# Optimization experiments

Measured on AMD Instinct MI355X. Metric: run time of the kernel, lower is better.

The kernel has to match this reference:

```python
import jax, jax.numpy as jnp
import numpy as np

B, N, C, H = 8, 1024, 768, 12
D = C // H
HID = 4 * C
MAX_TEXT_LEN = 512
LN_EPS = 1e-5


def _ln(x, g, b):
    mu = jnp.mean(x, axis=-1, keepdims=True)
    var = jnp.mean(jnp.square(x - mu), axis=-1, keepdims=True)
    return (x - mu) * jax.lax.rsqrt(var + LN_EPS) * g + b


def _mlp(x, w1, b1, w2, b2):
    h = jax.nn.gelu(x @ w1.T + b1, approximate=False)
    return h @ w2.T + b2


def setup_inputs() -> dict:
    key = jax.random.key(0)
    ks = jax.random.split(key, 16)
    s = 0.02
    return {
        "x": jax.random.normal(ks[0], (B, N, C), jnp.float32),
        "mask": jax.random.randint(ks[1], (B, N), 0, 2).astype(bool),
        "rel_bias": jax.random.normal(ks[2], (H, N, N), jnp.float32) * s,
        "w_qkv": jax.random.normal(ks[3], (3 * C, C), jnp.float32) * s,
        "q_bias": jnp.zeros((C,), jnp.float32),
        "v_bias": jnp.zeros((C,), jnp.float32),
        "w_proj": jax.random.normal(ks[4], (C, C), jnp.float32) * s,
        "b_proj": jnp.zeros((C,), jnp.float32),
        "ln1_g": jnp.ones((C,), jnp.float32),
        "ln1_b": jnp.zeros((C,), jnp.float32),
        "ln2t_g": jnp.ones((C,), jnp.float32),
        "ln2t_b": jnp.zeros((C,), jnp.float32),
        "ln2i_g": jnp.ones((C,), jnp.float32),
        "ln2i_b": jnp.zeros((C,), jnp.float32),
        "w1t": jax.random.normal(ks[5], (HID, C), jnp.float32) * s,
        "b1t": jnp.zeros((HID,), jnp.float32),
        "w2t": jax.random.normal(ks[6], (C, HID), jnp.float32) * s,
        "b2t": jnp.zeros((C,), jnp.float32),
        "w1i": jax.random.normal(ks[7], (HID, C), jnp.float32) * s,
        "b1i": jnp.zeros((HID,), jnp.float32),
        "w2i": jax.random.normal(ks[8], (C, HID), jnp.float32) * s,
        "b2i": jnp.zeros((C,), jnp.float32),
        "gamma1": jnp.full((C,), 0.1, jnp.float32),
        "gamma2": jnp.full((C,), 0.1, jnp.float32),
    }


def reference(x, mask, rel_bias, w_qkv, q_bias, v_bias, w_proj, b_proj,
              ln1_g, ln1_b, ln2t_g, ln2t_b, ln2i_g, ln2i_b,
              w1t, b1t, w2t, b2t, w1i, b1i, w2i, b2i, gamma1, gamma2):
    # ---- attention branch ----
    h = _ln(x, ln1_g, ln1_b)
    qkv_bias = jnp.concatenate([q_bias, jnp.zeros_like(v_bias), v_bias])
    qkv = h @ w_qkv.T + qkv_bias                      # [B,N,3C]
    qkv = qkv.reshape(B, N, 3, H, D).transpose(2, 0, 3, 1, 4)  # [3,B,H,N,D]
    q, k, v = qkv[0], qkv[1], qkv[2]
    q = q * (D ** -0.5)
    attn = jnp.einsum('bhnd,bhmd->bhnm',
                      q.astype(jnp.float32), k.astype(jnp.float32))
    attn = attn + rel_bias[None]                      # [B,H,N,N]
    attn = jnp.where(mask[:, None, None, :], attn, -jnp.inf)
    attn = jax.nn.softmax(attn, axis=-1).astype(x.dtype)
    out = jnp.einsum('bhnm,bhmd->bhnd', attn, v)
    out = out.transpose(0, 2, 1, 3).reshape(B, N, C)
    out = out @ w_proj.T + b_proj
    x = x + gamma1 * out
    # ---- dual-branch layer-scaled MLP (mlp_vl is None path) ----
    xt = x[:, :MAX_TEXT_LEN]
    xi = x[:, MAX_TEXT_LEN:]
    xt = xt + gamma2 * _mlp(_ln(xt, ln2t_g, ln2t_b), w1t, b1t, w2t, b2t)
    xi = xi + gamma2 * _mlp(_ln(xi, ln2i_g, ln2i_b), w1i, b1i, w2i, b2i)
    return jnp.concatenate([xt, xi], axis=1)
```

## Files before the change

kernel.cpp:

```cpp
#include <hip/hip_runtime.h>
#include <hip/hip_bf16.h>
#include <math.h>

#define B_    8
#define N_TOK 1024
#define C_    768
#define H_    12
#define D_    64
#define HID_  3072

typedef __attribute__((ext_vector_type(4)))  float f32x4;
typedef __attribute__((ext_vector_type(16))) float f32x16;
typedef __attribute__((ext_vector_type(8)))  short s16x8;
typedef __attribute__((ext_vector_type(4)))  unsigned short u16x4;

static __device__ __forceinline__ unsigned short f2bf(float x){
  union { __hip_bfloat16 h; unsigned short u; } cv;
  cv.h = __float2bfloat16(x);
  return cv.u;
}
static __device__ __forceinline__ float bf2f(unsigned short u){
  return __uint_as_float(((unsigned)u) << 16);
}

#define GLOAD_LDS16(gp, lp) \
  __builtin_amdgcn_global_load_lds((const __attribute__((address_space(1))) unsigned int*)(gp), \
                                   (__attribute__((address_space(3))) unsigned int*)(lp), 16, 0, 0)

__global__ __launch_bounds__(256) void k_cvtall(
    const float* __restrict__ wq,  const float* __restrict__ wp,
    const float* __restrict__ w1t, const float* __restrict__ w2t,
    const float* __restrict__ w1i, const float* __restrict__ w2i,
    const float* __restrict__ bias,
    unsigned short* __restrict__ dq,  unsigned short* __restrict__ dp,
    unsigned short* __restrict__ d1t, unsigned short* __restrict__ d2t,
    unsigned short* __restrict__ d1i, unsigned short* __restrict__ d2i,
    unsigned short* __restrict__ db)
{
  int i = blockIdx.x * 256 + threadIdx.x;
  const float* src; unsigned short* dst; int o;
  if      (i <  442368){ src = wq;  dst = dq;  o = i; }
  else if (i <  589824){ src = wp;  dst = dp;  o = i -  442368; }
  else if (i < 1179648){ src = w1t; dst = d1t; o = i -  589824; }
  else if (i < 1769472){ src = w2t; dst = d2t; o = i - 1179648; }
  else if (i < 2359296){ src = w1i; dst = d1i; o = i - 1769472; }
  else if (i < 2949120){ src = w2i; dst = d2i; o = i - 2359296; }
  else                 { src = bias;dst = db;  o = i - 2949120; }
  float4 v = ((const float4*)src)[o];
  u16x4 r;
  r.x = f2bf(v.x); r.y = f2bf(v.y); r.z = f2bf(v.z); r.w = f2bf(v.w);
  *(u16x4*)(dst + (size_t)o*4) = r;
}

__global__ __launch_bounds__(256) void k_ln1(const float* __restrict__ x,
                                             const float* __restrict__ g,
                                             const float* __restrict__ bta,
                                             unsigned short* __restrict__ out){
  int row  = blockIdx.x*4 + (threadIdx.x >> 6);
  int lane = threadIdx.x & 63;
  const float* xr = x + (size_t)row*C_;
  float v[12]; float s = 0.f;
  #pragma unroll
  for (int i=0;i<12;i++){ v[i] = xr[lane + i*64]; s += v[i]; }
  #pragma unroll
  for (int m=1;m<64;m<<=1) s += __shfl_xor(s, m);
  float mu = s * (1.f/768.f);
  float vs = 0.f;
  #pragma unroll
  for (int i=0;i<12;i++){ float d = v[i]-mu; vs += d*d; }
  #pragma unroll
  for (int m=1;m<64;m<<=1) vs += __shfl_xor(vs, m);
  float rs = rsqrtf(vs*(1.f/768.f) + 1e-5f);
  unsigned short* orow = out + (size_t)row*C_;
  #pragma unroll
  for (int i=0;i<12;i++){ int c = lane + i*64; orow[c] = f2bf((v[i]-mu)*rs*g[c] + bta[c]); }
}

__global__ __launch_bounds__(256) void k_ln2(const float* __restrict__ xmid,
                                             const float* __restrict__ gt, const float* __restrict__ bt,
                                             const float* __restrict__ gi, const float* __restrict__ bi,
                                             unsigned short* __restrict__ outc){
  int row  = blockIdx.x*4 + (threadIdx.x >> 6);
  int lane = threadIdx.x & 63;
  int bb = row >> 10, n = row & 1023;
  const float* G = (n < 512) ? gt : gi;
  const float* Bb = (n < 512) ? bt : bi;
  int crow = (n < 512) ? (bb*512 + n) : (4096 + bb*512 + (n - 512));
  const float* xr = xmid + (size_t)row*C_;
  float v[12]; float s = 0.f;
  #pragma unroll
  for (int i=0;i<12;i++){ v[i] = xr[lane + i*64]; s += v[i]; }
  #pragma unroll
  for (int m=1;m<64;m<<=1) s += __shfl_xor(s, m);
  float mu = s * (1.f/768.f);
  float vs = 0.f;
  #pragma unroll
  for (int i=0;i<12;i++){ float d = v[i]-mu; vs += d*d; }
  #pragma unroll
  for (int m=1;m<64;m<<=1) vs += __shfl_xor(vs, m);
  float rs = rsqrtf(vs*(1.f/768.f) + 1e-5f);
  unsigned short* orow = outc + (size_t)crow*C_;
  #pragma unroll
  for (int i=0;i<12;i++){ int c = lane + i*64; orow[c] = f2bf((v[i]-mu)*rs*G[c] + Bb[c]); }
}

template<int MODE>
__global__ __launch_bounds__(256, 3) void k_gemm2(
    const unsigned short* __restrict__ A,
    const unsigned short* __restrict__ Bw0,
    const unsigned short* __restrict__ Bw1,
    int K,
    const float* __restrict__ bias0,
    const float* __restrict__ bias1,
    const float* __restrict__ qb2,
    const float* __restrict__ resid,
    const float* __restrict__ gamma,
    unsigned short* __restrict__ out_bf,
    float* __restrict__ out_f)
{
  __shared__ __align__(16) char smem[49152];
  const int tid = threadIdx.x;
  const int lane = tid & 63, w = tid >> 6;
  const int wr = w >> 1, wc = w & 1;
  const int l31 = lane & 31, h5 = lane >> 5;

  const int gx = gridDim.x;
  const int nwg = gx * gridDim.y;
  const int flat = blockIdx.y * gx + blockIdx.x;
  const int nid = (flat & 7) * (nwg >> 3) + (flat >> 3);
  const int bx = nid % gx, by = nid / gx;
  const int z = blockIdx.z;
  const int row0 = bx*128, col0 = by*128;

  const unsigned short* Ap = A;
  const unsigned short* Bp = Bw0;
  const float* bias = bias0;
  if (MODE == 2 || MODE == 3){
    if (z){ Ap = A + (size_t)4096*K; Bp = Bw1; bias = bias1; }
  }
  const char* Abase = (const char*)Ap;
  const char* Bbase = (const char*)Bp;
  const size_t rowbytes = (size_t)K*2;
  const int KT2 = K >> 5;

  auto stage = [&](int h, int slot_idx){
    char* slot = smem + slot_idx*16384;
    size_t kb = (size_t)h*64;
    #pragma unroll
    for (int it = 0; it < 2; it++){
      int L = it*4096 + tid*16;
      int r = L >> 6, cb = L & 63;
      int scb = cb ^ ((r & 6) << 3);
      GLOAD_LDS16(Abase + (size_t)(row0 + r)*rowbytes + kb + scb, slot + L);
    }
    #pragma unroll
    for (int it = 0; it < 2; it++){
      int L = it*4096 + tid*16;
      int r = L >> 6, cb = L & 63;
      int scb = cb ^ ((r & 6) << 3);
      GLOAD_LDS16(Bbase + (size_t)(col0 + r)*rowbytes + kb + scb, slot + 8192 + L);
    }
  };

  stage(0, 0); stage(1, 1);
  asm volatile("s_waitcnt vmcnt(4)" ::: "memory");
  __builtin_amdgcn_s_barrier();

  f32x16 acc[2][2] = {};
  int sh = 2;
  int sc_ = 0;
  for (int h = 0; h < KT2; h++){
    if (h + 2 < KT2){
      stage(h + 2, sh);
      sh = (sh == 2) ? 0 : sh + 1;
    }
    char* slot = smem + sc_*16384;
    sc_ = (sc_ == 2) ? 0 : sc_ + 1;
    s16x8 af[2][2], bfr[2][2];
    #pragma unroll
    for (int fm = 0; fm < 2; fm++){
      int ra = wr*64 + fm*32 + l31;
      int swa = (ra & 6) << 3;
      af[fm][0] = *(const s16x8*)(slot + ra*64 + ((h5*16) ^ swa));
      af[fm][1] = *(const s16x8*)(slot + ra*64 + ((32 + h5*16) ^ swa));
    }
    #pragma unroll
    for (int fn = 0; fn < 2; fn++){
      int rb = wc*64 + fn*32 + l31;
      int swb = (rb & 6) << 3;
      bfr[fn][0] = *(const s16x8*)(slot + 8192 + rb*64 + ((h5*16) ^ swb));
      bfr[fn][1] = *(const s16x8*)(slot + 8192 + rb*64 + ((32 + h5*16) ^ swb));
    }
    __builtin_amdgcn_s_setprio(1);
    #pragma unroll
    for (int kh = 0; kh < 2; kh++)
      #pragma unroll
      for (int fm = 0; fm < 2; fm++)
        #pragma unroll
        for (int fn = 0; fn < 2; fn++)
          acc[fm][fn] = __builtin_amdgcn_mfma_f32_32x32x16_bf16(af[fm][kh], bfr[fn][kh], acc[fm][fn], 0, 0, 0);
    __builtin_amdgcn_s_setprio(0);
    if (h + 1 < KT2){
      if (h + 2 < KT2) asm volatile("s_waitcnt vmcnt(4)" ::: "memory");
      else             asm volatile("s_waitcnt vmcnt(0)" ::: "memory");
      __builtin_amdgcn_s_barrier();
    }
  }

  const float QSCALE = 0.18033688011f;
  #pragma unroll
  for (int fm = 0; fm < 2; fm++){
    #pragma unroll
    for (int fn = 0; fn < 2; fn++){
      int j = col0 + wc*64 + fn*32 + l31;
      f32x16 a = acc[fm][fn];
      if (MODE == 0){
        int which = (j >= 1536) ? 2 : (j >= 768 ? 1 : 0);
        int cj = j - which*768;
        float bs = (which == 0) ? bias0[cj] : (which == 2 ? qb2[cj] : 0.f);
        int head = cj >> 6, d = cj & 63;
        #pragma unroll
        for (int r = 0; r < 16; r++){
          int m = row0 + wr*64 + fm*32 + (r & 3) + 8*(r >> 2) + 4*h5;
          int bb = m >> 10, n = m & 1023;
          float val = a[r] + bs;
          if (which == 0) val *= QSCALE;
          out_bf[((((size_t)which*B_ + bb)*H_ + head)*N_TOK + n)*D_ + d] = f2bf(val);
        }
      } else if (MODE == 1){
        float gm = gamma[j], bs = bias[j];
        #pragma unroll
        for (int r = 0; r < 16; r++){
          int m = row0 + wr*64 + fm*32 + (r & 3) + 8*(r >> 2) + 4*h5;
          size_t idx = (size_t)m*C_ + j;
          out_f[idx] = resid[idx] + gm*(a[r] + bs);
        }
      } else if (MODE == 2){
        float bs = bias[j];
        unsigned short* outp = out_bf + (size_t)z*4096*HID_;
        #pragma unroll
        for (int r = 0; r < 16; r++){
          int m = row0 + wr*64 + fm*32 + (r & 3) + 8*(r >> 2) + 4*h5;
          float t = a[r] + bs;
          outp[(size_t)m*HID_ + j] = f2bf(0.5f*t*(1.f + erff(t*0.70710678118654752f)));
        }
      } else {
        float gm = gamma[j], bs = bias[j];
        #pragma unroll
        for (int r = 0; r < 16; r++){
          int m = row0 + wr*64 + fm*32 + (r & 3) + 8*(r >> 2) + 4*h5;
          int bb = m >> 9, n = (m & 511) + (z ? 512 : 0);
          size_t idx = ((size_t)bb*N_TOK + n)*C_ + j;
          out_f[idx] = resid[idx] + gm*(a[r] + bs);
        }
      }
    }
  }
}

__global__ __launch_bounds__(256, 2) void k_attn(
    const unsigned short* __restrict__ qb,
    const unsigned short* __restrict__ kb,
    const unsigned short* __restrict__ vb,
    const unsigned short* __restrict__ bias_bf,
    const int* __restrict__ mask,
    unsigned short* __restrict__ outb)
{
  __shared__ __align__(16) char smem[45056];
  char* Vt0 = smem;
  char* Vt1 = smem + 8192;
  char* Ks  = smem + 16384;
  char* Bs  = smem + 24576;
  float* maskf = (float*)(smem + 40960);
  char* Oep = smem;

  int wg = blockIdx.x;
  int x = wg & 7, rest = wg >> 3;
  int qt = rest & 7, gl = rest >> 3;
  int g = gl*8 + x;
  int h = g % 12, bb = g / 12;

  const int tid = threadIdx.x, lane = tid & 63, w = tid >> 6;
  const int l31 = lane & 31, h5 = lane >> 5;
  const size_t bh = (size_t)bb*H_ + h;
  const char* qp = (const char*)(qb + bh*N_TOK*D_);
  const char* kp = (const char*)(kb + bh*N_TOK*D_);
  const unsigned short* vp = vb + bh*N_TOK*D_;
  const char* bp = (const char*)(bias_bf + (size_t)h*N_TOK*N_TOK);
  const int q0 = qt*128;
  const int qrow = q0 + w*32 + l31;
  const int qr = w*32 + l31;

  #pragma unroll
  for (int it = 0; it < 2; it++){
    int L = it*4096 + tid*16; int r = L >> 7, cb = L & 127;
    GLOAD_LDS16(kp + (size_t)r*128 + (cb ^ ((r & 7) << 4)), Ks + L);
  }
  #pragma unroll
  for (int it = 0; it < 4; it++){
    int L = it*4096 + tid*16; int r = L >> 7, cb = L & 127;
    GLOAD_LDS16(bp + (size_t)(q0 + r)*2048 + (cb ^ ((r & 7) << 4)), Bs + L);
  }
  unsigned short vv[16];
  #pragma unroll
  for (int j = 0; j < 16; j++) vv[j] = vp[(size_t)(w*16 + j)*D_ + lane];
  {
    int4 m4 = *(const int4*)(mask + bb*N_TOK + tid*4);
    float4 f4;
    f4.x = m4.x ? 0.f : -1e30f; f4.y = m4.y ? 0.f : -1e30f;
    f4.z = m4.z ? 0.f : -1e30f; f4.w = m4.w ? 0.f : -1e30f;
    *(float4*)(maskf + tid*4) = f4;
  }
  s16x8 qf[4];
  #pragma unroll
  for (int t = 0; t < 4; t++)
    qf[t] = *(const s16x8*)(qp + (size_t)qrow*128 + t*32 + h5*16);
  #pragma unroll
  for (int i = 0; i < 2; i++){
    s16x8 pk;
    #pragma unroll
    for (int e = 0; e < 8; e++) pk[e] = (short)vv[i*8 + e];
    *(s16x8*)(Vt0 + lane*128 + ((w*32 + i*16) ^ ((lane & 7) << 4))) = pk;
  }
  __syncthreads();

  f32x16 oacc[2] = {};
  float lrow = 0.f;

  for (int t = 0; t < 16; t++){
    const int kt = t*64;
    char* Vbuf = (t & 1) ? Vt1 : Vt0;
    char* Vnxt = (t & 1) ? Vt0 : Vt1;

    s16x8 kfr[2][4];
    #pragma unroll
    for (int ck = 0; ck < 2; ck++)
      #pragma unroll
      for (int tt = 0; tt < 4; tt++)
        kfr[ck][tt] = *(const s16x8*)(Ks + (ck*32 + l31)*128 + ((tt*32 + h5*16) ^ ((l31 & 7) << 4)));
    u16x4 bv[2][4];
    #pragma unroll
    for (int ck = 0; ck < 2; ck++)
      #pragma unroll
      for (int rq = 0; rq < 4; rq++){
        int off = ck*64 + rq*16 + h5*8;
        bv[ck][rq] = *(const u16x4*)(Bs + qr*128 + (off ^ ((qr & 7) << 4)));
      }
    __syncthreads();

    if (t < 15){
      #pragma unroll
      for (int it = 0; it < 2; it++){
        int L = it*4096 + tid*16; int r = L >> 7, cb = L & 127;
        GLOAD_LDS16(kp + (size_t)(kt + 64 + r)*128 + (cb ^ ((r & 7) << 4)), Ks + L);
      }
      #pragma unroll
      for (int it = 0; it < 4; it++){
        int L = it*4096 + tid*16; int r = L >> 7, cb = L & 127;
        GLOAD_LDS16(bp + (size_t)(q0 + r)*2048 + (size_t)(kt + 64)*2 + (cb ^ ((r & 7) << 4)), Bs + L);
      }
      #pragma unroll
      for (int j = 0; j < 16; j++)
        vv[j] = vp[(size_t)(kt + 64 + w*16 + j)*D_ + lane];
    }

    f32x16 sacc[2] = {};
    __builtin_amdgcn_s_setprio(1);
    #pragma unroll
    for (int tt = 0; tt < 4; tt++){
      sacc[0] = __builtin_amdgcn_mfma_f32_32x32x16_bf16(kfr[0][tt], qf[tt], sacc[0], 0, 0, 0);
      sacc[1] = __builtin_amdgcn_mfma_f32_32x32x16_bf16(kfr[1][tt], qf[tt], sacc[1], 0, 0, 0);
    }
    __builtin_amdgcn_s_setprio(0);

    float sv[2][16];
    float ps = 0.f;
    #pragma unroll
    for (int ck = 0; ck < 2; ck++){
      #pragma unroll
      for (int r = 0; r < 16; r++){
        int kk = ck*32 + (r & 3) + 8*(r >> 2) + 4*h5;
        float p = exp2f(fmaf(bf2f(bv[ck][r >> 2][r & 3]), 1.44269504089f,
                             sacc[ck][r] + maskf[kt + kk]));
        sv[ck][r] = p;
        ps += p;
      }
    }
    lrow += ps;

    #pragma unroll
    for (int ck = 0; ck < 2; ck++){
      #pragma unroll
      for (int kh = 0; kh < 2; kh++){
        unsigned wA, wB, wC, wD;
        asm("v_cvt_pk_bf16_f32 %0, %1, %2" : "=v"(wA) : "v"(sv[ck][kh*8+0]), "v"(sv[ck][kh*8+1]));
        asm("v_cvt_pk_bf16_f32 %0, %1, %2" : "=v"(wB) : "v"(sv[ck][kh*8+2]), "v"(sv[ck][kh*8+3]));
        asm("v_cvt_pk_bf16_f32 %0, %1, %2" : "=v"(wC) : "v"(sv[ck][kh*8+4]), "v"(sv[ck][kh*8+5]));
        asm("v_cvt_pk_bf16_f32 %0, %1, %2" : "=v"(wD) : "v"(sv[ck][kh*8+6]), "v"(sv[ck][kh*8+7]));
        unsigned tA = (unsigned)__shfl_xor((int)wA, 32);
        unsigned tB = (unsigned)__shfl_xor((int)wB, 32);
        unsigned tC = (unsigned)__shfl_xor((int)wC, 32);
        unsigned tD = (unsigned)__shfl_xor((int)wD, 32);
        union { unsigned u[4]; s16x8 v; } pu;
        pu.u[0] = h5 ? tC : wA;
        pu.u[1] = h5 ? tD : wB;
        pu.u[2] = h5 ? wC : tA;
        pu.u[3] = h5 ? wD : tB;
        __builtin_amdgcn_s_setprio(1);
        #pragma unroll
        for (int dt = 0; dt < 2; dt++){
          int d = dt*32 + l31;
          s16x8 vf = *(const s16x8*)(Vbuf + d*128 + ((ck*64 + kh*32 + h5*16) ^ ((d & 7) << 4)));
          oacc[dt] = __builtin_amdgcn_mfma_f32_32x32x16_bf16(vf, pu.v, oacc[dt], 0, 0, 0);
        }
        __builtin_amdgcn_s_setprio(0);
      }
    }

    if (t < 15){
      #pragma unroll
      for (int i = 0; i < 2; i++){
        s16x8 pk;
        #pragma unroll
        for (int e = 0; e < 8; e++) pk[e] = (short)vv[i*8 + e];
        *(s16x8*)(Vnxt + lane*128 + ((w*32 + i*16) ^ ((lane & 7) << 4))) = pk;
      }
    }
    __syncthreads();
  }

  lrow += __shfl_xor(lrow, 32);
  float inv = 1.f / lrow;
  char* Ow = Oep + w*8192;
  #pragma unroll
  for (int dt = 0; dt < 2; dt++)
    #pragma unroll
    for (int r = 0; r < 16; r++){
      int d = dt*32 + (r & 3) + 8*(r >> 2) + 4*h5;
      *(float*)(Ow + l31*256 + ((d*4) ^ ((l31 & 7) << 4))) = oacc[dt][r] * inv;
    }
  int q2 = lane >> 1, dh = lane & 1;
  float of[32];
  #pragma unroll
  for (int i = 0; i < 8; i++){
    f32x4 v4 = *(const f32x4*)(Ow + q2*256 + ((dh*128 + i*16) ^ ((q2 & 7) << 4)));
    of[i*4+0] = v4[0]; of[i*4+1] = v4[1]; of[i*4+2] = v4[2]; of[i*4+3] = v4[3];
  }
  unsigned short* orow = outb + ((size_t)bb*N_TOK + q0 + w*32 + q2)*C_ + h*64 + dh*32;
  #pragma unroll
  for (int i = 0; i < 4; i++){
    s16x8 ob;
    #pragma unroll
    for (int e = 0; e < 8; e++) ob[e] = (short)f2bf(of[i*8+e]);
    *(s16x8*)(orow + i*8) = ob;
  }
}

extern "C" void kernel_launch(void* const* d_in, const int* in_sizes, int n_in,
                              void* d_out, int out_size, void* d_ws, size_t ws_size,
                              hipStream_t stream) {
  const float* x      = (const float*)d_in[0];
  const int*   mask   = (const int*)  d_in[1];
  const float* relb   = (const float*)d_in[2];
  const float* w_qkv  = (const float*)d_in[3];
  const float* q_bias = (const float*)d_in[4];
  const float* v_bias = (const float*)d_in[5];
  const float* w_proj = (const float*)d_in[6];
  const float* b_proj = (const float*)d_in[7];
  const float* ln1_g  = (const float*)d_in[8];
  const float* ln1_b  = (const float*)d_in[9];
  const float* ln2t_g = (const float*)d_in[10];
  const float* ln2t_b = (const float*)d_in[11];
  const float* ln2i_g = (const float*)d_in[12];
  const float* ln2i_b = (const float*)d_in[13];
  const float* w1t    = (const float*)d_in[14];
  const float* b1t    = (const float*)d_in[15];
  const float* w2t    = (const float*)d_in[16];
  const float* b2t    = (const float*)d_in[17];
  const float* w1i    = (const float*)d_in[18];
  const float* b1i    = (const float*)d_in[19];
  const float* w2i    = (const float*)d_in[20];
  const float* b2i    = (const float*)d_in[21];
  const float* gamma1 = (const float*)d_in[22];
  const float* gamma2 = (const float*)d_in[23];
  float* out = (float*)d_out;
  char* ws = (char*)d_ws;

  size_t off = 0;
  auto nxt = [&](size_t b){ size_t r = off; off += (b + 255) & ~(size_t)255; return r; };
  unsigned short* wq_bf  = (unsigned short*)(ws + nxt((size_t)3*C_*C_*2));
  unsigned short* wp_bf  = (unsigned short*)(ws + nxt((size_t)C_*C_*2));
  unsigned short* w1t_bf = (unsigned short*)(ws + nxt((size_t)HID_*C_*2));
  unsigned short* w2t_bf = (unsigned short*)(ws + nxt((size_t)HID_*C_*2));
  unsigned short* w1i_bf = (unsigned short*)(ws + nxt((size_t)HID_*C_*2));
  unsigned short* w2i_bf = (unsigned short*)(ws + nxt((size_t)HID_*C_*2));
  unsigned short* hln    = (unsigned short*)(ws + nxt((size_t)B_*N_TOK*C_*2));
  unsigned short* qkv    = (unsigned short*)(ws + nxt((size_t)3*B_*N_TOK*C_*2));
  unsigned short* attno  = (unsigned short*)(ws + nxt((size_t)B_*N_TOK*C_*2));
  float*          xmid   = (float*)(ws + nxt((size_t)B_*N_TOK*C_*4));
  unsigned short* ln2c   = hln;
  unsigned short* hidden = qkv;
  unsigned short* bias_bf = (unsigned short*)xmid;

  k_cvtall<<<dim3(23808), 256, 0, stream>>>(w_qkv, w_proj, w1t, w2t, w1i, w2i, relb,
                                            wq_bf, wp_bf, w1t_bf, w2t_bf, w1i_bf, w2i_bf, bias_bf);

  k_ln1<<<dim3(B_*N_TOK/4), 256, 0, stream>>>(x, ln1_g, ln1_b, hln);

  k_gemm2<0><<<dim3(64, 18, 1), 256, 0, stream>>>(hln, wq_bf, nullptr, C_,
                                                  q_bias, nullptr, v_bias,
                                                  nullptr, nullptr, qkv, nullptr);

  const size_t qsz = (size_t)B_*H_*N_TOK*D_;
  k_attn<<<dim3(768), 256, 0, stream>>>(qkv, qkv + qsz, qkv + 2*qsz, bias_bf, mask, attno);

  k_gemm2<1><<<dim3(64, 6, 1), 256, 0, stream>>>(attno, wp_bf, nullptr, C_,
                                                 b_proj, nullptr, nullptr,
                                                 x, gamma1, nullptr, xmid);

  k_ln2<<<dim3(B_*N_TOK/4), 256, 0, stream>>>(xmid, ln2t_g, ln2t_b, ln2i_g, ln2i_b, ln2c);

  k_gemm2<2><<<dim3(32, 24, 2), 256, 0, stream>>>(ln2c, w1t_bf, w1i_bf, C_,
                                                  b1t, b1i, nullptr,
                                                  nullptr, nullptr, hidden, nullptr);

  k_gemm2<3><<<dim3(32, 6, 2), 256, 0, stream>>>(hidden, w2t_bf, w2i_bf, HID_,
                                                 b2t, b2i, nullptr,
                                                 xmid, gamma2, nullptr, out);
}
```

Measured before the change: 328.8 us.

## Use 256x128 GEMM tiles with 512 threads for QKV and MLP-up

```diff
diff --git a/kernel.cpp b/kernel.cpp
--- a/kernel.cpp
+++ b/kernel.cpp
@@ -104,8 +104,8 @@
   for (int i=0;i<12;i++){ int c = lane + i*64; orow[c] = f2bf((v[i]-mu)*rs*G[c] + Bb[c]); }
 }
 
-template<int MODE>
-__global__ __launch_bounds__(256, 3) void k_gemm2(
+template<int MODE, int TM>
+__global__ __launch_bounds__(TM==256 ? 512 : 256, TM==256 ? 2 : 3) void k_gemm2(
     const unsigned short* __restrict__ A,
     const unsigned short* __restrict__ Bw0,
     const unsigned short* __restrict__ Bw1,
@@ -118,7 +118,11 @@
     unsigned short* __restrict__ out_bf,
     float* __restrict__ out_f)
 {
-  __shared__ __align__(16) char smem[49152];
+  constexpr int THREADS = (TM == 256) ? 512 : 256;
+  constexpr int ASLOT = TM * 64;
+  constexpr int SLOT  = ASLOT + 8192;
+  constexpr int BITS  = 8192 / (THREADS * 16);
+  __shared__ __align__(16) char smem[3 * SLOT];
   const int tid = threadIdx.x;
   const int lane = tid & 63, w = tid >> 6;
   const int wr = w >> 1, wc = w & 1;
@@ -130,7 +134,7 @@
   const int nid = (flat & 7) * (nwg >> 3) + (flat >> 3);
   const int bx = nid % gx, by = nid / gx;
   const int z = blockIdx.z;
-  const int row0 = bx*128, col0 = by*128;
+  const int row0 = bx*TM, col0 = by*128;
 
   const unsigned short* Ap = A;
   const unsigned short* Bp = Bw0;
@@ -144,37 +148,35 @@
   const int KT2 = K >> 5;
 
   auto stage = [&](int h, int slot_idx){
-    char* slot = smem + slot_idx*16384;
+    char* slot = smem + slot_idx*SLOT;
     size_t kb = (size_t)h*64;
     #pragma unroll
     for (int it = 0; it < 2; it++){
-      int L = it*4096 + tid*16;
+      int L = it*(THREADS*16) + tid*16;
       int r = L >> 6, cb = L & 63;
-      int scb = cb ^ ((r & 6) << 3);
-      GLOAD_LDS16(Abase + (size_t)(row0 + r)*rowbytes + kb + scb, slot + L);
-    }
-    #pragma unroll
-    for (int it = 0; it < 2; it++){
-      int L = it*4096 + tid*16;
+      GLOAD_LDS16(Abase + (size_t)(row0 + r)*rowbytes + kb + (cb ^ ((r & 6) << 3)), slot + L);
+    }
+    #pragma unroll
+    for (int it = 0; it < BITS; it++){
+      int L = it*(THREADS*16) + tid*16;
       int r = L >> 6, cb = L & 63;
-      int scb = cb ^ ((r & 6) << 3);
-      GLOAD_LDS16(Bbase + (size_t)(col0 + r)*rowbytes + kb + scb, slot + 8192 + L);
+      GLOAD_LDS16(Bbase + (size_t)(col0 + r)*rowbytes + kb + (cb ^ ((r & 6) << 3)), slot + ASLOT + L);
     }
   };
 
   stage(0, 0); stage(1, 1);
-  asm volatile("s_waitcnt vmcnt(4)" ::: "memory");
+  if constexpr (TM == 256) asm volatile("s_waitcnt vmcnt(3)" ::: "memory");
+  else                     asm volatile("s_waitcnt vmcnt(4)" ::: "memory");
   __builtin_amdgcn_s_barrier();
 
   f32x16 acc[2][2] = {};
-  int sh = 2;
-  int sc_ = 0;
+  int sh = 2, sc_ = 0;
   for (int h = 0; h < KT2; h++){
     if (h + 2 < KT2){
       stage(h + 2, sh);
       sh = (sh == 2) ? 0 : sh + 1;
     }
-    char* slot = smem + sc_*16384;
+    char* slot = smem + sc_*SLOT;
     sc_ = (sc_ == 2) ? 0 : sc_ + 1;
     s16x8 af[2][2], bfr[2][2];
     #pragma unroll
@@ -188,8 +190,8 @@
     for (int fn = 0; fn < 2; fn++){
       int rb = wc*64 + fn*32 + l31;
       int swb = (rb & 6) << 3;
-      bfr[fn][0] = *(const s16x8*)(slot + 8192 + rb*64 + ((h5*16) ^ swb));
-      bfr[fn][1] = *(const s16x8*)(slot + 8192 + rb*64 + ((32 + h5*16) ^ swb));
+      bfr[fn][0] = *(const s16x8*)(slot + ASLOT + rb*64 + ((h5*16) ^ swb));
+      bfr[fn][1] = *(const s16x8*)(slot + ASLOT + rb*64 + ((32 + h5*16) ^ swb));
     }
     __builtin_amdgcn_s_setprio(1);
     #pragma unroll
@@ -201,13 +203,16 @@
           acc[fm][fn] = __builtin_amdgcn_mfma_f32_32x32x16_bf16(af[fm][kh], bfr[fn][kh], acc[fm][fn], 0, 0, 0);
     __builtin_amdgcn_s_setprio(0);
     if (h + 1 < KT2){
-      if (h + 2 < KT2) asm volatile("s_waitcnt vmcnt(4)" ::: "memory");
-      else             asm volatile("s_waitcnt vmcnt(0)" ::: "memory");
+      if (h + 2 < KT2){
+        if constexpr (TM == 256) asm volatile("s_waitcnt vmcnt(3)" ::: "memory");
+        else                     asm volatile("s_waitcnt vmcnt(4)" ::: "memory");
+      } else {
+        asm volatile("s_waitcnt vmcnt(0)" ::: "memory");
+      }
       __builtin_amdgcn_s_barrier();
     }
   }
 
-  const float QSCALE = 0.18033688011f;
   #pragma unroll
   for (int fm = 0; fm < 2; fm++){
     #pragma unroll
@@ -224,7 +229,7 @@
           int m = row0 + wr*64 + fm*32 + (r & 3) + 8*(r >> 2) + 4*h5;
           int bb = m >> 10, n = m & 1023;
           float val = a[r] + bs;
-          if (which == 0) val *= QSCALE;
+          if (which == 0) val *= 0.125f;
           out_bf[((((size_t)which*B_ + bb)*H_ + head)*N_TOK + n)*D_ + d] = f2bf(val);
         }
       } else if (MODE == 1){
@@ -380,8 +385,7 @@
       #pragma unroll
       for (int r = 0; r < 16; r++){
         int kk = ck*32 + (r & 3) + 8*(r >> 2) + 4*h5;
-        float p = exp2f(fmaf(bf2f(bv[ck][r >> 2][r & 3]), 1.44269504089f,
-                             sacc[ck][r] + maskf[kt + kk]));
+        float p = __expf(sacc[ck][r] + bf2f(bv[ck][r >> 2][r & 3]) + maskf[kt + kk]);
         sv[ck][r] = p;
         ps += p;
       }
@@ -507,24 +511,24 @@
 
   k_ln1<<<dim3(B_*N_TOK/4), 256, 0, stream>>>(x, ln1_g, ln1_b, hln);
 
-  k_gemm2<0><<<dim3(64, 18, 1), 256, 0, stream>>>(hln, wq_bf, nullptr, C_,
-                                                  q_bias, nullptr, v_bias,
-                                                  nullptr, nullptr, qkv, nullptr);
+  k_gemm2<0,256><<<dim3(32, 18, 1), 512, 0, stream>>>(hln, wq_bf, nullptr, C_,
+                                                      q_bias, nullptr, v_bias,
+                                                      nullptr, nullptr, qkv, nullptr);
 
   const size_t qsz = (size_t)B_*H_*N_TOK*D_;
   k_attn<<<dim3(768), 256, 0, stream>>>(qkv, qkv + qsz, qkv + 2*qsz, bias_bf, mask, attno);
 
-  k_gemm2<1><<<dim3(64, 6, 1), 256, 0, stream>>>(attno, wp_bf, nullptr, C_,
-                                                 b_proj, nullptr, nullptr,
-                                                 x, gamma1, nullptr, xmid);
+  k_gemm2<1,128><<<dim3(64, 6, 1), 256, 0, stream>>>(attno, wp_bf, nullptr, C_,
+                                                     b_proj, nullptr, nullptr,
+                                                     x, gamma1, nullptr, xmid);
 
   k_ln2<<<dim3(B_*N_TOK/4), 256, 0, stream>>>(xmid, ln2t_g, ln2t_b, ln2i_g, ln2i_b, ln2c);
 
-  k_gemm2<2><<<dim3(32, 24, 2), 256, 0, stream>>>(ln2c, w1t_bf, w1i_bf, C_,
-                                                  b1t, b1i, nullptr,
-                                                  nullptr, nullptr, hidden, nullptr);
-
-  k_gemm2<3><<<dim3(32, 6, 2), 256, 0, stream>>>(hidden, w2t_bf, w2i_bf, HID_,
-                                                 b2t, b2i, nullptr,
-                                                 xmid, gamma2, nullptr, out);
-}
+  k_gemm2<2,256><<<dim3(16, 24, 2), 512, 0, stream>>>(ln2c, w1t_bf, w1i_bf, C_,
+                                                      b1t, b1i, nullptr,
+                                                      nullptr, nullptr, hidden, nullptr);
+
+  k_gemm2<3,128><<<dim3(32, 6, 2), 256, 0, stream>>>(hidden, w2t_bf, w2i_bf, HID_,
+                                                     b2t, b2i, nullptr,
+                                                     xmid, gamma2, nullptr, out);
+}
```

New measurement: 321.8 us. 2.1% less time.
